# Optimization experiments

Hardware: AMD Instinct MI355X
Metric: run time of the kernel (lower is better)

Reference implementation:

```python
import jax, jax.numpy as jnp
import numpy as np

EPS = 1e-8


def setup_inputs() -> dict:
    key = jax.random.key(0)
    k0, k1, k2, k3 = jax.random.split(key, 4)
    b, cin, cout, h, w, kk, cond = 16, 512, 512, 64, 64, 3, 512
    return {
        "x": jax.random.normal(k0, (b, cin, h, w), jnp.float32),
        "y": jax.random.normal(k1, (b, cond), jnp.float32),
        "w_conv": jax.random.normal(k2, (cout, cin, kk, kk), jnp.float32) * 0.05,
        "w_gamma": jax.random.normal(k3, (cin, cond), jnp.float32) * 0.05,
        "b_gamma": jnp.ones((cin,), jnp.float32),
    }


def reference(x, y, w_conv, w_gamma, b_gamma):
    # fc_gamma: per-sample per-input-channel modulation scale  [b, cin]
    gamma = y @ w_gamma.T + b_gamma
    # modulate: [b, cout, cin, kh, kw]
    weight = w_conv[None, :, :, :, :] * gamma[:, None, :, None, None]
    # demodulate: rsqrt of sum over (cin, kh, kw) per (b, cout)
    d = jax.lax.rsqrt(jnp.sum(weight * weight, axis=(2, 3, 4), keepdims=True) + EPS)
    weight = weight * d

    # per-sample conv (equivalent to groups=b grouped conv), stride 1, same padding
    def conv_one(xi, wi):
        # xi: [cin, h, w], wi: [cout, cin, kh, kw]
        out = jax.lax.conv_general_dilated(
            xi[None], wi, window_strides=(1, 1), padding=[(1, 1), (1, 1)],
            dimension_numbers=("NCHW", "OIHW", "NCHW"))
        return out[0]

    return jax.vmap(conv_one)(x, weight)  # [b, cout, h, w]
```

## Files before the change

### kernel.cpp

```cpp
#include <hip/hip_runtime.h>
#include <stdint.h>

#define NB   16
#define CIN  512
#define COUT 512
#define HH   64
#define WW   64
#define NCOND 512
#define TAPS 9
#define EPSD 1e-8f

typedef short bf16x8 __attribute__((ext_vector_type(8)));
typedef float f32x4 __attribute__((ext_vector_type(4)));

static __device__ __forceinline__ short f2bf(float f) {
  union { float f; uint32_t u; } c;
  c.f = f;
  uint32_t u = c.u;
  uint32_t r = (u + 0x7FFFu + ((u >> 16) & 1u)) >> 16;
  return (short)(uint16_t)r;
}

static __device__ __forceinline__ void gl_lds16(const void* g, void* l) {
  __builtin_amdgcn_global_load_lds(
      (const __attribute__((address_space(1))) void*)g,
      (__attribute__((address_space(3))) void*)l, 16, 0, 0);
}

__global__ __launch_bounds__(512) void k_gamma(const float* __restrict__ y,
                                               const float* __restrict__ w_gamma,
                                               const float* __restrict__ b_gamma,
                                               float* __restrict__ gamma,
                                               float* __restrict__ zbuf) {
  __shared__ float ys[NCOND];
  const int b = blockIdx.x;
  const int i = threadIdx.x;
  if (zbuf && b == 0) { zbuf[i] = 0.f; zbuf[i + 512] = 0.f; }
  ys[i] = y[b * NCOND + i];
  __syncthreads();
  const float4* wg = reinterpret_cast<const float4*>(w_gamma + (size_t)i * NCOND);
  float acc = b_gamma[i];
  for (int c4 = 0; c4 < NCOND / 4; ++c4) {
    float4 w4 = wg[c4];
    acc += w4.x * ys[c4 * 4 + 0] + w4.y * ys[c4 * 4 + 1] +
           w4.z * ys[c4 * 4 + 2] + w4.w * ys[c4 * 4 + 3];
  }
  gamma[b * CIN + i] = acc;
}

__global__ __launch_bounds__(256) void k_prep2(const float* __restrict__ w_conv,
                                               float* __restrict__ s2,
                                               short* __restrict__ W2) {
  __shared__ float ws_s[CIN * TAPS];
  const int o = blockIdx.x;
  const int t = threadIdx.x;
  const float* wsrc = w_conv + (size_t)o * CIN * TAPS;
  for (int idx = t; idx < CIN * TAPS; idx += 256) ws_s[idx] = wsrc[idx];
  __syncthreads();
  for (int i = t; i < CIN; i += 256) {
    float s = 0.f;
#pragma unroll
    for (int tap = 0; tap < TAPS; ++tap) {
      float v = ws_s[i * TAPS + tap];
      s += v * v;
    }
    s2[(size_t)o * CIN + i] = s;
  }
  const int key = (o >> 1) & 3;
  for (int k = t; k < CIN * TAPS; k += 256) {
    int tap = k >> 9;
    int r = k & 511;
    int c = r >> 5, sl = (r >> 3) & 3, j = r & 7;
    W2[((size_t)(c * TAPS + tap) * COUT + o) * 32 + ((sl ^ key) * 8) + j] =
        f2bf(ws_s[r * TAPS + tap]);
  }
}

__global__ __launch_bounds__(256) void k_prep(const float* __restrict__ w_conv,
                                              float* __restrict__ s2,
                                              short* __restrict__ Wr) {
  __shared__ float ws_s[CIN * TAPS];
  const int o = blockIdx.x;
  const int t = threadIdx.x;
  const float* wsrc = w_conv + (size_t)o * CIN * TAPS;
  for (int idx = t; idx < CIN * TAPS; idx += 256) ws_s[idx] = wsrc[idx];
  __syncthreads();
  for (int i = t; i < CIN; i += 256) {
    float s = 0.f;
#pragma unroll
    for (int tap = 0; tap < TAPS; ++tap) {
      float v = ws_s[i * TAPS + tap];
      s += v * v;
    }
    s2[(size_t)o * CIN + i] = s;
  }
  for (int idx = t; idx < CIN * TAPS; idx += 256) {
    int i = idx & (CIN - 1);
    int tap = idx >> 9;
    Wr[((size_t)o * TAPS + tap) * CIN + i] = f2bf(ws_s[i * TAPS + tap]);
  }
}

__global__ __launch_bounds__(512) void k_d(const float* __restrict__ gamma,
                                           const float* __restrict__ s2,
                                           float* __restrict__ dscale) {
  __shared__ float g2[CIN];
  const int b = blockIdx.x;
  const int o = threadIdx.x;
  float g = gamma[b * CIN + o];
  g2[o] = g * g;
  __syncthreads();
  const float4* s4 = reinterpret_cast<const float4*>(s2 + (size_t)o * CIN);
  float acc = 0.f;
  for (int i4 = 0; i4 < CIN / 4; ++i4) {
    float4 v = s4[i4];
    acc += v.x * g2[i4 * 4 + 0] + v.y * g2[i4 * 4 + 1] +
           v.z * g2[i4 * 4 + 2] + v.w * g2[i4 * 4 + 3];
  }
  dscale[b * COUT + o] = rsqrtf(acc + EPSD);
}

__global__ __launch_bounds__(256) void k_xmod2(const float* __restrict__ x,
                                               const float* __restrict__ gamma,
                                               short* __restrict__ xm) {
  __shared__ float tile[64][67];
  __shared__ float gs[CIN];
  const int y = blockIdx.x, b = blockIdx.y;
  const int t = threadIdx.x;
  gs[t] = gamma[b * CIN + t];
  gs[t + 256] = gamma[b * CIN + t + 256];
  __syncthreads();
  const int w = t >> 2, q = t & 3;
  const int sw = (w >> 1) & 3;
  short* dst = xm + (((size_t)b * HH + y) * WW + w) * CIN;
  for (int c0 = 0; c0 < CIN; c0 += 64) {
    {
      int ww_ = t & 63;
      int cb = t >> 6;
      const float* xp = x + (((size_t)(b * CIN + c0 + cb)) * HH + y) * WW + ww_;
#pragma unroll
      for (int p = 0; p < 16; ++p)
        tile[cb + p * 4][ww_] = xp[(size_t)p * 4 * HH * WW];
    }
    __syncthreads();
#pragma unroll
    for (int h = 0; h < 2; ++h) {
      int c_lo = q * 16 + h * 8;
      int chunk = (c0 + c_lo) >> 5;
      int sl = (c_lo >> 3) & 3;
      short tmp[8];
#pragma unroll
      for (int j = 0; j < 8; ++j)
        tmp[j] = f2bf(tile[c_lo + j][w] * gs[c0 + c_lo + j]);
      *reinterpret_cast<bf16x8*>(dst + chunk * 32 + (sl ^ sw) * 8) =
          *reinterpret_cast<const bf16x8*>(tmp);
    }
    __syncthreads();
  }
}

__global__ __launch_bounds__(512, 1) void k_conv6(const short* __restrict__ xm,
                                                  const short* __restrict__ W2,
                                                  const short* __restrict__ zbuf,
                                                  const float* __restrict__ dscale,
                                                  float* __restrict__ out) {
  __shared__ short As[4 * 256 * 32];
  __shared__ short Xs[2 * 6 * 64 * 32];
  __shared__ float d_s[256];
  __shared__ __align__(16) short zls[64];

  const int orig = blockIdx.x;
  const int wgid = ((orig & 7) << 6) | (orig >> 3);
  const int ot = wgid >> 8;
  const int b  = (wgid >> 4) & 15;
  const int sp = wgid & 15;

  const int t = threadIdx.x, lane = t & 63;
  const int wv = t >> 6;
  const int wr = wv >> 2;
  const int wc = wv & 3;
  const int l15 = lane & 15;
  const int kb0 = (lane >> 4) << 4;

  if (t < 256) d_s[t] = dscale[b * COUT + ot * 256 + t];
  if (t < 64) zls[t] = 0;

  const short* aS0 = W2 + (size_t)(ot * 256 + (t >> 2)) * 32 + (t & 3) * 8;
  const short* aS1 = aS0 + 128 * 32;
  const short* xS[3];
#pragma unroll
  for (int i = 0; i < 3; ++i) {
    int idx = t + 512 * i;
    int rb = idx >> 8;
    int w = (idx & 255) >> 2;
    int sl = idx & 3;
    int ysrc = sp * 4 + rb - 1;
    bool rv = (ysrc >= 0) && (ysrc < HH);
    xS[i] = rv ? xm + (((size_t)b * HH + ysrc) * WW + w) * CIN + sl * 8
               : zbuf + sl * 8;
  }

  const char* pa0 = (const char*)&As[0] + (wr * 128 + l15) * 64 +
                    (kb0 ^ (((l15 >> 1) & 3) << 4));
  const char* paR[4];
  char* waR[4];
#pragma unroll
  for (int i = 0; i < 4; ++i) {
    paR[i] = pa0 + i * 16384;
    waR[i] = (char*)&As[0] + t * 16 + i * 16384;
  }
  const char* pbx[3];
#pragma unroll
  for (int dxi = 0; dxi < 3; ++dxi) {
    int lcc = l15 + dxi - 1;
    int key = (lcc >> 1) & 3;
    pbx[dxi] = (const char*)&Xs[0] + lcc * 64 + (kb0 ^ (key << 4));
  }
  const int lc3 = (l15 + 1 > 15) ? 15 : (l15 + 1);
  const char* pbx3 = (const char*)&Xs[0] + lc3 * 64 + (kb0 ^ (((lc3 >> 1) & 3) << 4));
  char* wx0 = (char*)&Xs[0] + t * 16;
  const char* zl = (const char*)&zls[0];
  const bool mL = (l15 == 0);
  const bool mR = (l15 == 15);

  f32x4 acc[8][4];
#pragma unroll
  for (int m = 0; m < 8; ++m)
#pragma unroll
    for (int n = 0; n < 4; ++n)
      acc[m][n] = (f32x4){0.f, 0.f, 0.f, 0.f};

#pragma unroll
  for (int i = 0; i < 3; ++i)
    gl_lds16(xS[i], wx0 + i * 8192);
#pragma unroll
  for (int s = 0; s < 3; ++s) {
    gl_lds16(aS0 + s * 16384, waR[s]);
    gl_lds16(aS1 + s * 16384, waR[s] + 8192);
  }
  asm volatile("s_waitcnt vmcnt(0) lgkmcnt(0)" ::: "memory");
  __builtin_amdgcn_s_barrier();
  asm volatile("" ::: "memory");

  int chBase = 0;
  int kx = 0;
  uint32_t xb = 0;

  for (int ch = 0; ch < 16; ++ch) {
    const int advA = (ch < 15) ? 9 * 16384 : 0;
    const int kn = (ch < 15) ? kx + 32 : 0;
    const char* q0 = pbx[0] + xb;
    const char* q1 = pbx[1] + xb;
    const char* q2 = pbx[2] + xb;
    const char* q3 = pbx3 + xb;
    char* wxT = wx0 + (xb ^ 24576);

#pragma unroll
    for (int tp = 0; tp < TAPS; ++tp) {
      const int dy = tp / 3 - 1, dx = tp % 3 - 1;
      const int rbo = (wc + dy + 1) * 4096;

      bf16x8 afr[4], af2[4], bfr[4];
#pragma unroll
      for (int m = 0; m < 4; ++m)
        afr[m] = *reinterpret_cast<const bf16x8*>(paR[tp & 3] + m * 1024);
      {
        const char* qq = (dx == -1) ? q0 : ((dx == 0) ? q1 : q2);
        const char* s0 = (dx == -1 && mL) ? (zl - rbo) : qq;
        const char* s3 = (dx == 1) ? (mR ? (zl - rbo - 3 * 1024) : q3) : qq;
        bfr[0] = *reinterpret_cast<const bf16x8*>(s0 + rbo);
        bfr[1] = *reinterpret_cast<const bf16x8*>(qq + rbo + 1024);
        bfr[2] = *reinterpret_cast<const bf16x8*>(qq + rbo + 2048);
        bfr[3] = *reinterpret_cast<const bf16x8*>(s3 + rbo + 3072);
      }
      __builtin_amdgcn_sched_barrier(0);
#pragma unroll
      for (int m = 0; m < 4; ++m)
        af2[m] = *reinterpret_cast<const bf16x8*>(paR[tp & 3] + (4 + m) * 1024);

      if (tp == 7) {
#pragma unroll
        for (int i = 0; i < 3; ++i)
          gl_lds16(xS[i] + kn, wxT + i * 8192);
      }
      {
        const int pan = chBase + ((tp >= 6) ? advA : 0) + ((tp + 3) % 9) * 16384;
        gl_lds16(aS0 + pan, waR[(tp + 3) & 3]);
        gl_lds16(aS1 + pan, waR[(tp + 3) & 3] + 8192);
      }

      asm volatile("s_waitcnt lgkmcnt(4)" ::: "memory");
      __builtin_amdgcn_sched_barrier(0);
      __builtin_amdgcn_s_setprio(1);
#pragma unroll
      for (int m = 0; m < 4; ++m)
#pragma unroll
        for (int n = 0; n < 4; ++n)
          acc[m][n] = __builtin_amdgcn_mfma_f32_16x16x32_bf16(afr[m], bfr[n],
                                                              acc[m][n], 0, 0, 0);
      asm volatile("s_waitcnt lgkmcnt(0)" ::: "memory");
      __builtin_amdgcn_sched_barrier(0);
#pragma unroll
      for (int m = 0; m < 4; ++m)
#pragma unroll
        for (int n = 0; n < 4; ++n)
          acc[4 + m][n] = __builtin_amdgcn_mfma_f32_16x16x32_bf16(af2[m], bfr[n],
                                                                  acc[4 + m][n], 0, 0, 0);
      __builtin_amdgcn_s_setprio(0);
      if (tp == 7) {
        asm volatile("s_waitcnt vmcnt(7)" ::: "memory");
      } else {
        asm volatile("s_waitcnt vmcnt(4)" ::: "memory");
      }
      __builtin_amdgcn_s_barrier();
      asm volatile("" ::: "memory");
    }
    {
      const char* tA = paR[0];
      paR[0] = paR[1]; paR[1] = paR[2]; paR[2] = paR[3]; paR[3] = tA;
      char* tW = waR[0];
      waR[0] = waR[1]; waR[1] = waR[2]; waR[2] = waR[3]; waR[3] = tW;
    }
    chBase += 9 * 16384;
    kx += 32;
    xb ^= 24576;
  }

  asm volatile("s_waitcnt vmcnt(0)" ::: "memory");
  __builtin_amdgcn_s_barrier();

#pragma unroll
  for (int m = 0; m < 8; ++m) {
#pragma unroll
    for (int n = 0; n < 4; ++n) {
#pragma unroll
      for (int j = 0; j < 4; ++j) {
        int o_l = wr * 128 + m * 16 + (lane >> 4) * 4 + j;
        int o = ot * 256 + o_l;
        int yy = sp * 4 + wc;
        int cx = n * 16 + l15;
        out[(((size_t)b * COUT + o) * HH + yy) * WW + cx] = d_s[o_l] * acc[m][n][j];
      }
    }
  }
}

__global__ __launch_bounds__(256) void k_conv_fb(const float* __restrict__ x,
                                                 const short* __restrict__ Wr,
                                                 const float* __restrict__ gamma,
                                                 const float* __restrict__ dscale,
                                                 float* __restrict__ out) {
  __shared__ short As[128 * 64];
  __shared__ short Xs[4 * 64 * 64];
  __shared__ float gam_s[CIN];
  __shared__ float d_s[128];

  const int sp = blockIdx.x;
  const int ot = blockIdx.y;
  const int b  = blockIdx.z;
  const int t  = threadIdx.x;
  const int lane = t & 63;
  const int wv = t >> 6;
  const int wr = wv >> 1;
  const int wc = wv & 1;

  gam_s[t] = gamma[b * CIN + t];
  gam_s[t + 256] = gamma[b * CIN + t + 256];
  if (t < 128) d_s[t] = dscale[b * COUT + ot * 128 + t];

  f32x4 acc[4][4];
#pragma unroll
  for (int m = 0; m < 4; ++m)
#pragma unroll
    for (int n = 0; n < 4; ++n)
      acc[m][n] = (f32x4){0.f, 0.f, 0.f, 0.f};

  const int srow = t >> 6;
  const int sc = t & 63;
  const int ysrc = sp * 2 + srow - 1;
  const bool rv = (ysrc >= 0) && (ysrc < HH);
  const int ycl = rv ? ysrc : 0;
  const float* xrow = x + (((size_t)b * CIN) * HH + ycl) * WW + sc;
  short* xs_base = &Xs[(srow * 64 + sc) * 64];
  const int xs_sw = (sc & 7) << 4;

  for (int chunk = 0; chunk < CIN / 64; ++chunk) {
    const int i0 = chunk * 64;
    __syncthreads();
    {
      const float* xp = xrow + (size_t)i0 * (HH * WW);
#pragma unroll
      for (int i8 = 0; i8 < 8; ++i8) {
        short tmp[8];
#pragma unroll
        for (int j = 0; j < 8; ++j) {
          int i = i8 * 8 + j;
          float v = rv ? xp[i * (HH * WW)] : 0.0f;
          tmp[j] = f2bf(v * gam_s[i0 + i]);
        }
        char* dst = (char*)xs_base + ((i8 * 16) ^ xs_sw);
        *reinterpret_cast<bf16x8*>(dst) = *reinterpret_cast<const bf16x8*>(tmp);
      }
    }
    for (int tap = 0; tap < TAPS; ++tap) {
      __syncthreads();
#pragma unroll
      for (int j = 0; j < 4; ++j) {
        int s = t + 256 * j;
        int row = s >> 3, sl = s & 7;
        int kbyte = (sl * 16) ^ ((row & 7) << 4);
        const short* src = Wr + ((size_t)(ot * 128 + row) * TAPS + tap) * CIN +
                           i0 + (kbyte >> 1);
        *reinterpret_cast<bf16x8*>((char*)As + row * 128 + sl * 16) =
            *reinterpret_cast<const bf16x8*>(src);
      }
      __syncthreads();

      const int dy = tap / 3 - 1, dx = tap % 3 - 1;
      bf16x8 afr[2][4], bfr[2][4];
#pragma unroll
      for (int kk = 0; kk < 2; ++kk) {
        const int kb = kk * 64 + (lane >> 4) * 16;
#pragma unroll
        for (int m = 0; m < 4; ++m) {
          int row = wr * 64 + m * 16 + (lane & 15);
          afr[kk][m] = *reinterpret_cast<const bf16x8*>(
              (const char*)As + row * 128 + (kb ^ ((row & 7) << 4)));
        }
#pragma unroll
        for (int n = 0; n < 4; ++n) {
          int p = wc * 64 + n * 16 + (lane & 15);
          int r = p >> 6, c = p & 63;
          int cc = c + dx;
          bool val = (cc >= 0) && (cc < WW);
          int ccl = val ? cc : 0;
          int rr = r + dy + 1;
          bf16x8 f = *reinterpret_cast<const bf16x8*>(
              (const char*)Xs + (rr * 64 + ccl) * 128 + (kb ^ ((ccl & 7) << 4)));
          if (!val) f = (bf16x8){0, 0, 0, 0, 0, 0, 0, 0};
          bfr[kk][n] = f;
        }
      }
#pragma unroll
      for (int m = 0; m < 4; ++m)
#pragma unroll
        for (int n = 0; n < 4; ++n)
#pragma unroll
          for (int kk = 0; kk < 2; ++kk)
            acc[m][n] = __builtin_amdgcn_mfma_f32_16x16x32_bf16(
                afr[kk][m], bfr[kk][n], acc[m][n], 0, 0, 0);
    }
  }

#pragma unroll
  for (int m = 0; m < 4; ++m) {
#pragma unroll
    for (int n = 0; n < 4; ++n) {
#pragma unroll
      for (int j = 0; j < 4; ++j) {
        int o_l = wr * 64 + m * 16 + (lane >> 4) * 4 + j;
        int o = ot * 128 + o_l;
        int p = wc * 64 + n * 16 + (lane & 15);
        int yy = sp * 2 + (p >> 6);
        int cx = p & 63;
        out[(((size_t)b * COUT + o) * HH + yy) * WW + cx] = d_s[o_l] * acc[m][n][j];
      }
    }
  }
}

extern "C" void kernel_launch(void* const* d_in, const int* in_sizes, int n_in,
                              void* d_out, int out_size, void* d_ws, size_t ws_size,
                              hipStream_t stream) {
  const float* x = (const float*)d_in[0];
  const float* y = (const float*)d_in[1];
  const float* w_conv = (const float*)d_in[2];
  const float* w_gamma = (const float*)d_in[3];
  const float* b_gamma = (const float*)d_in[4];
  float* out = (float*)d_out;

  char* ws = (char*)d_ws;
  short* W2 = (short*)ws;
  float* gamma = (float*)(ws + 4849664);
  float* dsc = (float*)(ws + 4882432);
  float* s2 = (float*)(ws + 4915200);
  char* zbuf = ws + 5963776;
  short* xm = (short*)(ws + 5967872);
  const size_t NEED = 5967872 + (size_t)NB * HH * WW * CIN * 2 + 4096;

  const bool fast = ws_size >= NEED;

  if (fast) {
    hipLaunchKernelGGL(k_gamma, dim3(NB), dim3(512), 0, stream, y, w_gamma,
                       b_gamma, gamma, (float*)zbuf);
    hipLaunchKernelGGL(k_prep2, dim3(COUT), dim3(256), 0, stream, w_conv, s2, W2);
    hipLaunchKernelGGL(k_d, dim3(NB), dim3(512), 0, stream, gamma, s2, dsc);
    hipLaunchKernelGGL(k_xmod2, dim3(HH, NB), dim3(256), 0, stream, x, gamma, xm);
    hipLaunchKernelGGL(k_conv6, dim3(512), dim3(512), 0, stream, xm, W2,
                       (const short*)zbuf, dsc, out);
  } else {
    hipLaunchKernelGGL(k_gamma, dim3(NB), dim3(512), 0, stream, y, w_gamma,
                       b_gamma, gamma, (float*)nullptr);
    hipLaunchKernelGGL(k_prep, dim3(COUT), dim3(256), 0, stream, w_conv, s2, W2);
    hipLaunchKernelGGL(k_d, dim3(NB), dim3(512), 0, stream, gamma, s2, dsc);
    hipLaunchKernelGGL(k_conv_fb, dim3(32, 4, NB), dim3(256), 0, stream, x, W2,
                       gamma, dsc, out);
  }
}
```

Baseline: 330.0 us.

## Halve conv workgroup waves, doubling per-wave output tile to 256x32 pixels

The conv kernel now runs 4 waves per workgroup instead of 8. Each wave covers two output rows (8 N-fragments) instead of one, so the accumulator doubles to 8x8 MFMA tiles. Each A fragment read from LDS now feeds twice as many MFMAs, which cuts LDS traffic per FLOP, and each thread issues more global-to-LDS loads. The risks are high register pressure from 256 accumulator VGPRs and fewer waves to hide latency.

```diff
diff --git a/kernel.cpp b/kernel.cpp
--- a/kernel.cpp
+++ b/kernel.cpp
@@ -159,7 +159,7 @@
   }
 }
 
-__global__ __launch_bounds__(512, 1) void k_conv6(const short* __restrict__ xm,
+__global__ __launch_bounds__(256, 1) void k_conv7(const short* __restrict__ xm,
                                                   const short* __restrict__ W2,
                                                   const short* __restrict__ zbuf,
                                                   const float* __restrict__ dscale,
@@ -177,20 +177,25 @@
 
   const int t = threadIdx.x, lane = t & 63;
   const int wv = t >> 6;
-  const int wr = wv >> 2;
-  const int wc = wv & 3;
+  const int wr = wv >> 1;
+  const int wp = wv & 1;
   const int l15 = lane & 15;
   const int kb0 = (lane >> 4) << 4;
-
-  if (t < 256) d_s[t] = dscale[b * COUT + ot * 256 + t];
+  const int wpo = wp * 8192;
+
+  d_s[t] = dscale[b * COUT + ot * 256 + t];
   if (t < 64) zls[t] = 0;
 
-  const short* aS0 = W2 + (size_t)(ot * 256 + (t >> 2)) * 32 + (t & 3) * 8;
-  const short* aS1 = aS0 + 128 * 32;
-  const short* xS[3];
-#pragma unroll
-  for (int i = 0; i < 3; ++i) {
-    int idx = t + 512 * i;
+  const short* aSr[4];
+#pragma unroll
+  for (int i = 0; i < 4; ++i) {
+    int s = t + 256 * i;
+    aSr[i] = W2 + (size_t)(ot * 256 + (s >> 2)) * 32 + (s & 3) * 8;
+  }
+  const short* xS[6];
+#pragma unroll
+  for (int i = 0; i < 6; ++i) {
+    int idx = t + 256 * i;
     int rb = idx >> 8;
     int w = (idx & 255) >> 2;
     int sl = idx & 3;
@@ -223,21 +228,21 @@
   const bool mL = (l15 == 0);
   const bool mR = (l15 == 15);
 
-  f32x4 acc[8][4];
+  f32x4 acc[8][8];
 #pragma unroll
   for (int m = 0; m < 8; ++m)
 #pragma unroll
-    for (int n = 0; n < 4; ++n)
+    for (int n = 0; n < 8; ++n)
       acc[m][n] = (f32x4){0.f, 0.f, 0.f, 0.f};
 
 #pragma unroll
-  for (int i = 0; i < 3; ++i)
-    gl_lds16(xS[i], wx0 + i * 8192);
-#pragma unroll
-  for (int s = 0; s < 3; ++s) {
-    gl_lds16(aS0 + s * 16384, waR[s]);
-    gl_lds16(aS1 + s * 16384, waR[s] + 8192);
-  }
+  for (int i = 0; i < 6; ++i)
+    gl_lds16(xS[i], wx0 + i * 4096);
+#pragma unroll
+  for (int s = 0; s < 3; ++s)
+#pragma unroll
+    for (int i = 0; i < 4; ++i)
+      gl_lds16(aSr[i] + s * 16384, waR[s] + i * 4096);
   asm volatile("s_waitcnt vmcnt(0) lgkmcnt(0)" ::: "memory");
   __builtin_amdgcn_s_barrier();
   asm volatile("" ::: "memory");
@@ -249,29 +254,32 @@
   for (int ch = 0; ch < 16; ++ch) {
     const int advA = (ch < 15) ? 9 * 16384 : 0;
     const int kn = (ch < 15) ? kx + 32 : 0;
-    const char* q0 = pbx[0] + xb;
-    const char* q1 = pbx[1] + xb;
-    const char* q2 = pbx[2] + xb;
-    const char* q3 = pbx3 + xb;
+    const char* q0 = pbx[0] + xb + wpo;
+    const char* q1 = pbx[1] + xb + wpo;
+    const char* q2 = pbx[2] + xb + wpo;
+    const char* q3 = pbx3 + xb + wpo;
     char* wxT = wx0 + (xb ^ 24576);
 
 #pragma unroll
     for (int tp = 0; tp < TAPS; ++tp) {
       const int dy = tp / 3 - 1, dx = tp % 3 - 1;
-      const int rbo = (wc + dy + 1) * 4096;
-
-      bf16x8 afr[4], af2[4], bfr[4];
+
+      bf16x8 afr[4], af2[4], bfr[8];
 #pragma unroll
       for (int m = 0; m < 4; ++m)
         afr[m] = *reinterpret_cast<const bf16x8*>(paR[tp & 3] + m * 1024);
-      {
-        const char* qq = (dx == -1) ? q0 : ((dx == 0) ? q1 : q2);
-        const char* s0 = (dx == -1 && mL) ? (zl - rbo) : qq;
-        const char* s3 = (dx == 1) ? (mR ? (zl - rbo - 3 * 1024) : q3) : qq;
-        bfr[0] = *reinterpret_cast<const bf16x8*>(s0 + rbo);
-        bfr[1] = *reinterpret_cast<const bf16x8*>(qq + rbo + 1024);
-        bfr[2] = *reinterpret_cast<const bf16x8*>(qq + rbo + 2048);
-        bfr[3] = *reinterpret_cast<const bf16x8*>(s3 + rbo + 3072);
+#pragma unroll
+      for (int n = 0; n < 8; ++n) {
+        const int g = n & 3;
+        const int rbo = ((n >> 2) + dy + 1) * 4096;
+        const char* srcn;
+        if (dx == -1 && g == 0)
+          srcn = mL ? (zl - rbo) : q0;
+        else if (dx == 1 && g == 3)
+          srcn = mR ? (zl - rbo - 3 * 1024) : q3;
+        else
+          srcn = (dx == -1) ? q0 : ((dx == 0) ? q1 : q2);
+        bfr[n] = *reinterpret_cast<const bf16x8*>(srcn + rbo + g * 1024);
       }
       __builtin_amdgcn_sched_barrier(0);
 #pragma unroll
@@ -280,13 +288,14 @@
 
       if (tp == 7) {
 #pragma unroll
-        for (int i = 0; i < 3; ++i)
-          gl_lds16(xS[i] + kn, wxT + i * 8192);
+        for (int i = 0; i < 6; ++i)
+          gl_lds16(xS[i] + kn, wxT + i * 4096);
       }
       {
         const int pan = chBase + ((tp >= 6) ? advA : 0) + ((tp + 3) % 9) * 16384;
-        gl_lds16(aS0 + pan, waR[(tp + 3) & 3]);
-        gl_lds16(aS1 + pan, waR[(tp + 3) & 3] + 8192);
+#pragma unroll
+        for (int i = 0; i < 4; ++i)
+          gl_lds16(aSr[i] + pan, waR[(tp + 3) & 3] + i * 4096);
       }
 
       asm volatile("s_waitcnt lgkmcnt(4)" ::: "memory");
@@ -295,7 +304,7 @@
 #pragma unroll
       for (int m = 0; m < 4; ++m)
 #pragma unroll
-        for (int n = 0; n < 4; ++n)
+        for (int n = 0; n < 8; ++n)
           acc[m][n] = __builtin_amdgcn_mfma_f32_16x16x32_bf16(afr[m], bfr[n],
                                                               acc[m][n], 0, 0, 0);
       asm volatile("s_waitcnt lgkmcnt(0)" ::: "memory");
@@ -303,14 +312,14 @@
 #pragma unroll
       for (int m = 0; m < 4; ++m)
 #pragma unroll
-        for (int n = 0; n < 4; ++n)
+        for (int n = 0; n < 8; ++n)
           acc[4 + m][n] = __builtin_amdgcn_mfma_f32_16x16x32_bf16(af2[m], bfr[n],
                                                                   acc[4 + m][n], 0, 0, 0);
       __builtin_amdgcn_s_setprio(0);
       if (tp == 7) {
-        asm volatile("s_waitcnt vmcnt(7)" ::: "memory");
+        asm volatile("s_waitcnt vmcnt(10)" ::: "memory");
       } else {
-        asm volatile("s_waitcnt vmcnt(4)" ::: "memory");
+        asm volatile("s_waitcnt vmcnt(8)" ::: "memory");
       }
       __builtin_amdgcn_s_barrier();
       asm volatile("" ::: "memory");
@@ -332,13 +341,13 @@
 #pragma unroll
   for (int m = 0; m < 8; ++m) {
 #pragma unroll
-    for (int n = 0; n < 4; ++n) {
+    for (int n = 0; n < 8; ++n) {
 #pragma unroll
       for (int j = 0; j < 4; ++j) {
         int o_l = wr * 128 + m * 16 + (lane >> 4) * 4 + j;
         int o = ot * 256 + o_l;
-        int yy = sp * 4 + wc;
-        int cx = n * 16 + l15;
+        int yy = sp * 4 + wp * 2 + (n >> 2);
+        int cx = (n & 3) * 16 + l15;
         out[(((size_t)b * COUT + o) * HH + yy) * WW + cx] = d_s[o_l] * acc[m][n][j];
       }
     }
@@ -496,7 +505,7 @@
     hipLaunchKernelGGL(k_prep2, dim3(COUT), dim3(256), 0, stream, w_conv, s2, W2);
     hipLaunchKernelGGL(k_d, dim3(NB), dim3(512), 0, stream, gamma, s2, dsc);
     hipLaunchKernelGGL(k_xmod2, dim3(HH, NB), dim3(256), 0, stream, x, gamma, xm);
-    hipLaunchKernelGGL(k_conv6, dim3(512), dim3(512), 0, stream, xm, W2,
+    hipLaunchKernelGGL(k_conv7, dim3(512), dim3(256), 0, stream, xm, W2,
                        (const short*)zbuf, dsc, out);
   } else {
     hipLaunchKernelGGL(k_gamma, dim3(NB), dim3(512), 0, stream, y, w_gamma,
```

After: 406.5 us. 23.2% more time.

## Load conv weight fragments directly from global into registers, drop LDS staging

Applied to the files above, without the earlier changes.

The weight operand is no longer staged through a 4-slot LDS ring. Each wave now loads its A fragments straight from global memory into double-buffered registers (aA/aB), prefetching the next tap while the current tap's MFMAs run. This frees 64KB of LDS and removes most per-tap barriers, leaving one barrier per channel chunk, and the launch bound is raised to two blocks per CU. In exchange it adds many more per-wave global loads of weights, which are shared across waves and were previously deduplicated by LDS. The added 64 VGPRs of double-buffered fragments also risk register spills under the tighter 2-block bound.

```diff
diff --git a/kernel.cpp b/kernel.cpp
--- a/kernel.cpp
+++ b/kernel.cpp
@@ -159,12 +159,11 @@
   }
 }
 
-__global__ __launch_bounds__(512, 1) void k_conv6(const short* __restrict__ xm,
+__global__ __launch_bounds__(512, 2) void k_conv8(const short* __restrict__ xm,
                                                   const short* __restrict__ W2,
                                                   const short* __restrict__ zbuf,
                                                   const float* __restrict__ dscale,
                                                   float* __restrict__ out) {
-  __shared__ short As[4 * 256 * 32];
   __shared__ short Xs[2 * 6 * 64 * 32];
   __shared__ float d_s[256];
   __shared__ __align__(16) short zls[64];
@@ -180,13 +179,11 @@
   const int wr = wv >> 2;
   const int wc = wv & 3;
   const int l15 = lane & 15;
-  const int kb0 = (lane >> 4) << 4;
+  const int slA = lane >> 4;
 
   if (t < 256) d_s[t] = dscale[b * COUT + ot * 256 + t];
   if (t < 64) zls[t] = 0;
 
-  const short* aS0 = W2 + (size_t)(ot * 256 + (t >> 2)) * 32 + (t & 3) * 8;
-  const short* aS1 = aS0 + 128 * 32;
   const short* xS[3];
 #pragma unroll
   for (int i = 0; i < 3; ++i) {
@@ -200,15 +197,11 @@
                : zbuf + sl * 8;
   }
 
-  const char* pa0 = (const char*)&As[0] + (wr * 128 + l15) * 64 +
-                    (kb0 ^ (((l15 >> 1) & 3) << 4));
-  const char* paR[4];
-  char* waR[4];
-#pragma unroll
-  for (int i = 0; i < 4; ++i) {
-    paR[i] = pa0 + i * 16384;
-    waR[i] = (char*)&As[0] + t * 16 + i * 16384;
-  }
+  const int o0 = ot * 256 + wr * 128 + l15;
+  const int keyA = (o0 >> 1) & 3;
+  const short* aGc = W2 + (size_t)o0 * 32 + ((slA ^ keyA) * 8);
+
+  const int kb0 = slA << 4;
   const char* pbx[3];
 #pragma unroll
   for (int dxi = 0; dxi < 3; ++dxi) {
@@ -230,104 +223,88 @@
     for (int n = 0; n < 4; ++n)
       acc[m][n] = (f32x4){0.f, 0.f, 0.f, 0.f};
 
+  bf16x8 aA[8], aB[8];
+
 #pragma unroll
   for (int i = 0; i < 3; ++i)
     gl_lds16(xS[i], wx0 + i * 8192);
 #pragma unroll
-  for (int s = 0; s < 3; ++s) {
-    gl_lds16(aS0 + s * 16384, waR[s]);
-    gl_lds16(aS1 + s * 16384, waR[s] + 8192);
-  }
+  for (int m = 0; m < 8; ++m)
+    aA[m] = *reinterpret_cast<const bf16x8*>(aGc + m * 512);
   asm volatile("s_waitcnt vmcnt(0) lgkmcnt(0)" ::: "memory");
   __builtin_amdgcn_s_barrier();
   asm volatile("" ::: "memory");
 
-  int chBase = 0;
-  int kx = 0;
-  uint32_t xb = 0;
-
-  for (int ch = 0; ch < 16; ++ch) {
-    const int advA = (ch < 15) ? 9 * 16384 : 0;
-    const int kn = (ch < 15) ? kx + 32 : 0;
-    const char* q0 = pbx[0] + xb;
-    const char* q1 = pbx[1] + xb;
-    const char* q2 = pbx[2] + xb;
-    const char* q3 = pbx3 + xb;
-    char* wxT = wx0 + (xb ^ 24576);
-
-#pragma unroll
-    for (int tp = 0; tp < TAPS; ++tp) {
-      const int dy = tp / 3 - 1, dx = tp % 3 - 1;
-      const int rbo = (wc + dy + 1) * 4096;
-
-      bf16x8 afr[4], af2[4], bfr[4];
-#pragma unroll
-      for (int m = 0; m < 4; ++m)
-        afr[m] = *reinterpret_cast<const bf16x8*>(paR[tp & 3] + m * 1024);
-      {
-        const char* qq = (dx == -1) ? q0 : ((dx == 0) ? q1 : q2);
-        const char* s0 = (dx == -1 && mL) ? (zl - rbo) : qq;
-        const char* s3 = (dx == 1) ? (mR ? (zl - rbo - 3 * 1024) : q3) : qq;
-        bfr[0] = *reinterpret_cast<const bf16x8*>(s0 + rbo);
-        bfr[1] = *reinterpret_cast<const bf16x8*>(qq + rbo + 1024);
-        bfr[2] = *reinterpret_cast<const bf16x8*>(qq + rbo + 2048);
-        bfr[3] = *reinterpret_cast<const bf16x8*>(s3 + rbo + 3072);
-      }
-      __builtin_amdgcn_sched_barrier(0);
-#pragma unroll
-      for (int m = 0; m < 4; ++m)
-        af2[m] = *reinterpret_cast<const bf16x8*>(paR[tp & 3] + (4 + m) * 1024);
-
-      if (tp == 7) {
-#pragma unroll
-        for (int i = 0; i < 3; ++i)
-          gl_lds16(xS[i] + kn, wxT + i * 8192);
-      }
-      {
-        const int pan = chBase + ((tp >= 6) ? advA : 0) + ((tp + 3) % 9) * 16384;
-        gl_lds16(aS0 + pan, waR[(tp + 3) & 3]);
-        gl_lds16(aS1 + pan, waR[(tp + 3) & 3] + 8192);
-      }
-
-      asm volatile("s_waitcnt lgkmcnt(4)" ::: "memory");
-      __builtin_amdgcn_sched_barrier(0);
-      __builtin_amdgcn_s_setprio(1);
-#pragma unroll
-      for (int m = 0; m < 4; ++m)
-#pragma unroll
-        for (int n = 0; n < 4; ++n)
-          acc[m][n] = __builtin_amdgcn_mfma_f32_16x16x32_bf16(afr[m], bfr[n],
-                                                              acc[m][n], 0, 0, 0);
-      asm volatile("s_waitcnt lgkmcnt(0)" ::: "memory");
-      __builtin_amdgcn_sched_barrier(0);
-#pragma unroll
-      for (int m = 0; m < 4; ++m)
-#pragma unroll
-        for (int n = 0; n < 4; ++n)
-          acc[4 + m][n] = __builtin_amdgcn_mfma_f32_16x16x32_bf16(af2[m], bfr[n],
-                                                                  acc[4 + m][n], 0, 0, 0);
-      __builtin_amdgcn_s_setprio(0);
-      if (tp == 7) {
-        asm volatile("s_waitcnt vmcnt(7)" ::: "memory");
-      } else {
-        asm volatile("s_waitcnt vmcnt(4)" ::: "memory");
-      }
-      __builtin_amdgcn_s_barrier();
-      asm volatile("" ::: "memory");
-    }
+#define DO_TAP(tp, CUR, NXT, NXTOFF, STGX, KNV)                               \
+  {                                                                           \
+    const short* an_ = aGc + (NXTOFF);                                        \
+    _Pragma("unroll") for (int m_ = 0; m_ < 8; ++m_)                          \
+        NXT[m_] = *reinterpret_cast<const bf16x8*>(an_ + m_ * 512);           \
+    if (STGX) {                                                               \
+      _Pragma("unroll") for (int i_ = 0; i_ < 3; ++i_)                        \
+          gl_lds16(xS[i_] + (KNV), wxw + i_ * 8192);                          \
+    }                                                                         \
+    __builtin_amdgcn_sched_barrier(0);                                        \
+    {                                                                         \
+      const int dy_ = (tp) / 3 - 1, dx_ = (tp) % 3 - 1;                       \
+      const int rbo_ = (wc + dy_ + 1) * 4096;                                 \
+      bf16x8 bfr[4];                                                          \
+      const char* qq_ = (dx_ == -1) ? qq0 : ((dx_ == 0) ? qq1 : qq2);         \
+      const char* s0_ = (dx_ == -1 && mL) ? (zl - rbo_) : qq_;                \
+      const char* s3_ = (dx_ == 1) ? (mR ? (zl - rbo_ - 3072) : qq3) : qq_;   \
+      bfr[0] = *reinterpret_cast<const bf16x8*>(s0_ + rbo_);                  \
+      bfr[1] = *reinterpret_cast<const bf16x8*>(qq_ + rbo_ + 1024);           \
+      bfr[2] = *reinterpret_cast<const bf16x8*>(qq_ + rbo_ + 2048);           \
+      bfr[3] = *reinterpret_cast<const bf16x8*>(s3_ + rbo_ + 3072);           \
+      __builtin_amdgcn_s_setprio(1);                                          \
+      _Pragma("unroll") for (int m_ = 0; m_ < 8; ++m_)                        \
+        _Pragma("unroll") for (int n_ = 0; n_ < 4; ++n_)                      \
+          acc[m_][n_] = __builtin_amdgcn_mfma_f32_16x16x32_bf16(              \
+              CUR[m_], bfr[n_], acc[m_][n_], 0, 0, 0);                        \
+      __builtin_amdgcn_s_setprio(0);                                          \
+    }                                                                         \
+  }
+
+#define CHUNK_TAPS(A0, A1, NX8, KNV)                                          \
+  DO_TAP(0, A0, A1, 16384, false, 0)                                          \
+  DO_TAP(1, A1, A0, 32768, false, 0)                                          \
+  DO_TAP(2, A0, A1, 49152, false, 0)                                          \
+  DO_TAP(3, A1, A0, 65536, false, 0)                                          \
+  DO_TAP(4, A0, A1, 81920, false, 0)                                          \
+  DO_TAP(5, A1, A0, 98304, false, 0)                                          \
+  DO_TAP(6, A0, A1, 114688, false, 0)                                         \
+  DO_TAP(7, A1, A0, 131072, true, KNV)                                        \
+  DO_TAP(8, A0, A1, (NX8), false, 0)                                          \
+  __builtin_amdgcn_sched_barrier(0);                                          \
+  asm volatile("s_waitcnt vmcnt(8)" ::: "memory");                            \
+  __builtin_amdgcn_s_barrier();                                               \
+  asm volatile("" ::: "memory");
+
+  for (int c2 = 0; c2 < 8; ++c2) {
     {
-      const char* tA = paR[0];
-      paR[0] = paR[1]; paR[1] = paR[2]; paR[2] = paR[3]; paR[3] = tA;
-      char* tW = waR[0];
-      waR[0] = waR[1]; waR[1] = waR[2]; waR[2] = waR[3]; waR[3] = tW;
-    }
-    chBase += 9 * 16384;
-    kx += 32;
-    xb ^= 24576;
-  }
-
-  asm volatile("s_waitcnt vmcnt(0)" ::: "memory");
-  __builtin_amdgcn_s_barrier();
+      const char* qq0 = pbx[0];
+      const char* qq1 = pbx[1];
+      const char* qq2 = pbx[2];
+      const char* qq3 = pbx3;
+      char* wxw = wx0 + 24576;
+      const int knv = (2 * c2 + 1) * 32;
+      CHUNK_TAPS(aA, aB, 147456, knv)
+    }
+    aGc += 147456;
+    {
+      const char* qq0 = pbx[0] + 24576;
+      const char* qq1 = pbx[1] + 24576;
+      const char* qq2 = pbx[2] + 24576;
+      const char* qq3 = pbx3 + 24576;
+      char* wxw = wx0;
+      const int knv = (c2 < 7) ? (2 * c2 + 2) * 32 : 0;
+      const int nx8 = (c2 < 7) ? 147456 : 0;
+      CHUNK_TAPS(aB, aA, nx8, knv)
+    }
+    aGc += 147456;
+  }
+#undef CHUNK_TAPS
+#undef DO_TAP
 
 #pragma unroll
   for (int m = 0; m < 8; ++m) {
@@ -496,7 +473,7 @@
     hipLaunchKernelGGL(k_prep2, dim3(COUT), dim3(256), 0, stream, w_conv, s2, W2);
     hipLaunchKernelGGL(k_d, dim3(NB), dim3(512), 0, stream, gamma, s2, dsc);
     hipLaunchKernelGGL(k_xmod2, dim3(HH, NB), dim3(256), 0, stream, x, gamma, xm);
-    hipLaunchKernelGGL(k_conv6, dim3(512), dim3(512), 0, stream, xm, W2,
+    hipLaunchKernelGGL(k_conv8, dim3(512), dim3(512), 0, stream, xm, W2,
                        (const short*)zbuf, dsc, out);
   } else {
     hipLaunchKernelGGL(k_gamma, dim3(NB), dim3(512), 0, stream, y, w_gamma,
```

Result: no change. 335.8 us (+1.8%).

## Double-buffer MFMA fragments across taps and fuse gamma with demod kernel

Applied to the files above, without the earlier changes.

The conv main loop now prefetches the next tap's A and B register fragments (ping-pong fa0/fa1, fb0/fb1) while issuing 32 MFMAs on the current tap, replacing the split 16+16 MFMA scheme that waited on LDS loads mid-tap. Chunks are unrolled in pairs so the register buffers alternate statically, and the waitcnt thresholds are retuned. Separately, the gamma and demodulation-scale kernels are fused into one launch to drop a kernel boundary. The prefetching roughly doubles the fragment registers held live, which adds register pressure in a kernel already limited to one workgroup per CU.

```diff
diff --git a/kernel.cpp b/kernel.cpp
--- a/kernel.cpp
+++ b/kernel.cpp
@@ -48,6 +48,40 @@
   gamma[b * CIN + i] = acc;
 }
 
+__global__ __launch_bounds__(512) void k_gd(const float* __restrict__ y,
+                                            const float* __restrict__ w_gamma,
+                                            const float* __restrict__ b_gamma,
+                                            const float* __restrict__ s2,
+                                            float* __restrict__ gamma,
+                                            float* __restrict__ dscale,
+                                            float* __restrict__ zbuf) {
+  __shared__ float ys[NCOND];
+  __shared__ float g2[CIN];
+  const int b = blockIdx.x;
+  const int i = threadIdx.x;
+  if (b == 0) { zbuf[i] = 0.f; zbuf[i + 512] = 0.f; }
+  ys[i] = y[b * NCOND + i];
+  __syncthreads();
+  const float4* wg = reinterpret_cast<const float4*>(w_gamma + (size_t)i * NCOND);
+  float acc = b_gamma[i];
+  for (int c4 = 0; c4 < NCOND / 4; ++c4) {
+    float4 w4 = wg[c4];
+    acc += w4.x * ys[c4 * 4 + 0] + w4.y * ys[c4 * 4 + 1] +
+           w4.z * ys[c4 * 4 + 2] + w4.w * ys[c4 * 4 + 3];
+  }
+  gamma[b * CIN + i] = acc;
+  g2[i] = acc * acc;
+  __syncthreads();
+  const float4* s4 = reinterpret_cast<const float4*>(s2 + (size_t)i * CIN);
+  float a2 = 0.f;
+  for (int c4 = 0; c4 < CIN / 4; ++c4) {
+    float4 v = s4[c4];
+    a2 += v.x * g2[c4 * 4 + 0] + v.y * g2[c4 * 4 + 1] +
+          v.z * g2[c4 * 4 + 2] + v.w * g2[c4 * 4 + 3];
+  }
+  dscale[b * COUT + i] = rsqrtf(a2 + EPSD);
+}
+
 __global__ __launch_bounds__(256) void k_prep2(const float* __restrict__ w_conv,
                                                float* __restrict__ s2,
                                                short* __restrict__ W2) {
@@ -159,11 +193,11 @@
   }
 }
 
-__global__ __launch_bounds__(512, 1) void k_conv6(const short* __restrict__ xm,
-                                                  const short* __restrict__ W2,
-                                                  const short* __restrict__ zbuf,
-                                                  const float* __restrict__ dscale,
-                                                  float* __restrict__ out) {
+__global__ __launch_bounds__(512, 1) void k_conv10(const short* __restrict__ xm,
+                                                   const short* __restrict__ W2,
+                                                   const short* __restrict__ zbuf,
+                                                   const float* __restrict__ dscale,
+                                                   float* __restrict__ out) {
   __shared__ short As[4 * 256 * 32];
   __shared__ short Xs[2 * 6 * 64 * 32];
   __shared__ float d_s[256];
@@ -230,6 +264,76 @@
     for (int n = 0; n < 4; ++n)
       acc[m][n] = (f32x4){0.f, 0.f, 0.f, 0.f};
 
+  bf16x8 fa0[8], fb0[4], fa1[8], fb1[4];
+
+#define LD8(p) (*reinterpret_cast<const bf16x8*>(p))
+
+#define LOAD_A(FA, tpn)                                                  \
+  { _Pragma("unroll") for (int m_ = 0; m_ < 8; ++m_)                     \
+      FA[m_] = LD8(paR[(tpn) & 3] + m_ * 1024); }
+
+#define LOAD_B(FB, tpn)                                                  \
+  { const int dy_ = (tpn) / 3 - 1, dx_ = (tpn) % 3 - 1;                  \
+    const int rbo_ = (wc + dy_ + 1) * 4096;                              \
+    const char* qq_ = (dx_ == -1) ? q0 : ((dx_ == 0) ? q1 : q2);         \
+    const char* s0_ = (dx_ == -1 && mL) ? (zl - rbo_) : qq_;             \
+    const char* s3_ = (dx_ == 1) ? (mR ? (zl - rbo_ - 3072) : q3) : qq_; \
+    FB[0] = LD8(s0_ + rbo_);                                             \
+    FB[1] = LD8(qq_ + rbo_ + 1024);                                      \
+    FB[2] = LD8(qq_ + rbo_ + 2048);                                      \
+    FB[3] = LD8(s3_ + rbo_ + 3072); }
+
+#define MFMA32(CA, CB)                                                   \
+  { __builtin_amdgcn_s_setprio(1);                                       \
+    _Pragma("unroll") for (int m_ = 0; m_ < 8; ++m_)                     \
+      _Pragma("unroll") for (int n_ = 0; n_ < 4; ++n_)                   \
+        acc[m_][n_] = __builtin_amdgcn_mfma_f32_16x16x32_bf16(           \
+            CA[m_], CB[n_], acc[m_][n_], 0, 0, 0);                       \
+    __builtin_amdgcn_s_setprio(0); }
+
+#define DO_TAP(tp, CA, CB, NA, NB_)                                      \
+  { const int pan_ = chBase + ((tp) >= 6 ? advA : 0) +                   \
+                     (((tp) + 3) % 9) * 16384;                           \
+    gl_lds16(aS0 + pan_, waR[((tp) + 3) & 3]);                           \
+    gl_lds16(aS1 + pan_, waR[((tp) + 3) & 3] + 8192); }                  \
+  if ((tp) == 7) {                                                       \
+    _Pragma("unroll") for (int i_ = 0; i_ < 3; ++i_)                     \
+        gl_lds16(xS[i_] + knv, wxT + i_ * 8192);                         \
+  }                                                                      \
+  if ((tp) < 8) {                                                        \
+    LOAD_A(NA, (tp) + 1)                                                 \
+    LOAD_B(NB_, (tp) + 1)                                                \
+    asm volatile("s_waitcnt lgkmcnt(12)" ::: "memory");                  \
+  } else {                                                               \
+    LOAD_A(NA, 9)                                                        \
+    asm volatile("s_waitcnt lgkmcnt(8)" ::: "memory");                   \
+  }                                                                      \
+  __builtin_amdgcn_sched_barrier(0);                                     \
+  MFMA32(CA, CB)                                                         \
+  if ((tp) == 7) { asm volatile("s_waitcnt vmcnt(5)" ::: "memory"); }    \
+  else { asm volatile("s_waitcnt vmcnt(2)" ::: "memory"); }              \
+  __builtin_amdgcn_s_barrier();                                          \
+  asm volatile("" ::: "memory");
+
+#define RUN_CHUNK(FAS, FBS, FAO, FBO)                                    \
+  LOAD_B(FBS, 0)                                                         \
+  DO_TAP(0, FAS, FBS, FAO, FBO)                                          \
+  DO_TAP(1, FAO, FBO, FAS, FBS)                                          \
+  DO_TAP(2, FAS, FBS, FAO, FBO)                                          \
+  DO_TAP(3, FAO, FBO, FAS, FBS)                                          \
+  DO_TAP(4, FAS, FBS, FAO, FBO)                                          \
+  DO_TAP(5, FAO, FBO, FAS, FBS)                                          \
+  DO_TAP(6, FAS, FBS, FAO, FBO)                                          \
+  DO_TAP(7, FAO, FBO, FAS, FBS)                                          \
+  DO_TAP(8, FAS, FBS, FAO, FBO)
+
+#define ROT_RING()                                                       \
+  { const char* tA_ = paR[0];                                            \
+    paR[0] = paR[1]; paR[1] = paR[2]; paR[2] = paR[3]; paR[3] = tA_;     \
+    char* tW_ = waR[0];                                                  \
+    waR[0] = waR[1]; waR[1] = waR[2]; waR[2] = waR[3]; waR[3] = tW_;     \
+    chBase += 9 * 16384; xb ^= 24576; }
+
 #pragma unroll
   for (int i = 0; i < 3; ++i)
     gl_lds16(xS[i], wx0 + i * 8192);
@@ -241,90 +345,42 @@
   asm volatile("s_waitcnt vmcnt(0) lgkmcnt(0)" ::: "memory");
   __builtin_amdgcn_s_barrier();
   asm volatile("" ::: "memory");
+  LOAD_A(fa0, 0)
 
   int chBase = 0;
-  int kx = 0;
   uint32_t xb = 0;
 
-  for (int ch = 0; ch < 16; ++ch) {
-    const int advA = (ch < 15) ? 9 * 16384 : 0;
-    const int kn = (ch < 15) ? kx + 32 : 0;
-    const char* q0 = pbx[0] + xb;
-    const char* q1 = pbx[1] + xb;
-    const char* q2 = pbx[2] + xb;
-    const char* q3 = pbx3 + xb;
-    char* wxT = wx0 + (xb ^ 24576);
-
-#pragma unroll
-    for (int tp = 0; tp < TAPS; ++tp) {
-      const int dy = tp / 3 - 1, dx = tp % 3 - 1;
-      const int rbo = (wc + dy + 1) * 4096;
-
-      bf16x8 afr[4], af2[4], bfr[4];
-#pragma unroll
-      for (int m = 0; m < 4; ++m)
-        afr[m] = *reinterpret_cast<const bf16x8*>(paR[tp & 3] + m * 1024);
-      {
-        const char* qq = (dx == -1) ? q0 : ((dx == 0) ? q1 : q2);
-        const char* s0 = (dx == -1 && mL) ? (zl - rbo) : qq;
-        const char* s3 = (dx == 1) ? (mR ? (zl - rbo - 3 * 1024) : q3) : qq;
-        bfr[0] = *reinterpret_cast<const bf16x8*>(s0 + rbo);
-        bfr[1] = *reinterpret_cast<const bf16x8*>(qq + rbo + 1024);
-        bfr[2] = *reinterpret_cast<const bf16x8*>(qq + rbo + 2048);
-        bfr[3] = *reinterpret_cast<const bf16x8*>(s3 + rbo + 3072);
-      }
-      __builtin_amdgcn_sched_barrier(0);
-#pragma unroll
-      for (int m = 0; m < 4; ++m)
-        af2[m] = *reinterpret_cast<const bf16x8*>(paR[tp & 3] + (4 + m) * 1024);
-
-      if (tp == 7) {
-#pragma unroll
-        for (int i = 0; i < 3; ++i)
-          gl_lds16(xS[i] + kn, wxT + i * 8192);
-      }
-      {
-        const int pan = chBase + ((tp >= 6) ? advA : 0) + ((tp + 3) % 9) * 16384;
-        gl_lds16(aS0 + pan, waR[(tp + 3) & 3]);
-        gl_lds16(aS1 + pan, waR[(tp + 3) & 3] + 8192);
-      }
-
-      asm volatile("s_waitcnt lgkmcnt(4)" ::: "memory");
-      __builtin_amdgcn_sched_barrier(0);
-      __builtin_amdgcn_s_setprio(1);
-#pragma unroll
-      for (int m = 0; m < 4; ++m)
-#pragma unroll
-        for (int n = 0; n < 4; ++n)
-          acc[m][n] = __builtin_amdgcn_mfma_f32_16x16x32_bf16(afr[m], bfr[n],
-                                                              acc[m][n], 0, 0, 0);
-      asm volatile("s_waitcnt lgkmcnt(0)" ::: "memory");
-      __builtin_amdgcn_sched_barrier(0);
-#pragma unroll
-      for (int m = 0; m < 4; ++m)
-#pragma unroll
-        for (int n = 0; n < 4; ++n)
-          acc[4 + m][n] = __builtin_amdgcn_mfma_f32_16x16x32_bf16(af2[m], bfr[n],
-                                                                  acc[4 + m][n], 0, 0, 0);
-      __builtin_amdgcn_s_setprio(0);
-      if (tp == 7) {
-        asm volatile("s_waitcnt vmcnt(7)" ::: "memory");
-      } else {
-        asm volatile("s_waitcnt vmcnt(4)" ::: "memory");
-      }
-      __builtin_amdgcn_s_barrier();
-      asm volatile("" ::: "memory");
-    }
+  for (int c2 = 0; c2 < 8; ++c2) {
     {
-      const char* tA = paR[0];
-      paR[0] = paR[1]; paR[1] = paR[2]; paR[2] = paR[3]; paR[3] = tA;
-      char* tW = waR[0];
-      waR[0] = waR[1]; waR[1] = waR[2]; waR[2] = waR[3]; waR[3] = tW;
-    }
-    chBase += 9 * 16384;
-    kx += 32;
-    xb ^= 24576;
-  }
+      const int advA = 9 * 16384;
+      const int knv = (2 * c2 + 1) * 32;
+      const char* q0 = pbx[0] + xb;
+      const char* q1 = pbx[1] + xb;
+      const char* q2 = pbx[2] + xb;
+      const char* q3 = pbx3 + xb;
+      char* wxT = wx0 + (xb ^ 24576);
+      RUN_CHUNK(fa0, fb0, fa1, fb1)
+      ROT_RING()
+    }
+    {
+      const int advA = (c2 < 7) ? 9 * 16384 : 0;
+      const int knv = (c2 < 7) ? (2 * c2 + 2) * 32 : 0;
+      const char* q0 = pbx[0] + xb;
+      const char* q1 = pbx[1] + xb;
+      const char* q2 = pbx[2] + xb;
+      const char* q3 = pbx3 + xb;
+      char* wxT = wx0 + (xb ^ 24576);
+      RUN_CHUNK(fa1, fb1, fa0, fb0)
+      ROT_RING()
+    }
+  }
+#undef ROT_RING
+#undef RUN_CHUNK
+#undef DO_TAP
+#undef MFMA32
+#undef LOAD_B
+#undef LOAD_A
+#undef LD8
 
   asm volatile("s_waitcnt vmcnt(0)" ::: "memory");
   __builtin_amdgcn_s_barrier();
@@ -491,12 +547,11 @@
   const bool fast = ws_size >= NEED;
 
   if (fast) {
-    hipLaunchKernelGGL(k_gamma, dim3(NB), dim3(512), 0, stream, y, w_gamma,
-                       b_gamma, gamma, (float*)zbuf);
     hipLaunchKernelGGL(k_prep2, dim3(COUT), dim3(256), 0, stream, w_conv, s2, W2);
-    hipLaunchKernelGGL(k_d, dim3(NB), dim3(512), 0, stream, gamma, s2, dsc);
+    hipLaunchKernelGGL(k_gd, dim3(NB), dim3(512), 0, stream, y, w_gamma, b_gamma,
+                       s2, gamma, dsc, (float*)zbuf);
     hipLaunchKernelGGL(k_xmod2, dim3(HH, NB), dim3(256), 0, stream, x, gamma, xm);
-    hipLaunchKernelGGL(k_conv6, dim3(512), dim3(512), 0, stream, xm, W2,
+    hipLaunchKernelGGL(k_conv10, dim3(512), dim3(512), 0, stream, xm, W2,
                        (const short*)zbuf, dsc, out);
   } else {
     hipLaunchKernelGGL(k_gamma, dim3(NB), dim3(512), 0, stream, y, w_gamma,
```

Result: slower. 402.3 us (+21.9%).
